# Kernel optimization log

Hardware: AMD Instinct MI355X
Metric: run time of the kernel (lower is better)

Reference implementation:

```python
import jax, jax.numpy as jnp
import numpy as np


def _l2norm(x, axis=1, eps=1e-12):
    n = jnp.sqrt(jnp.sum(x * x, axis=axis, keepdims=True))
    return x / jnp.maximum(n, eps)


def _update(query, keys, labels, class_counts, num_classes):
    # Vectorized form of Memory.update + get_update_query (train branch).
    m, d = keys.shape
    q = _l2norm(query, axis=1)                              # [N, d]
    score = q @ keys.T                                      # [N, m]
    s_q = jax.nn.softmax(score, axis=0)                     # softmax over queries
    s_m = jax.nn.softmax(score, axis=1)                     # softmax over memory slots
    gather = jnp.argmax(s_m, axis=1)                        # top-1 slot per query, [N]
    # per-slot scatter-reduce: sum_{i: argmax_i==j} s_q[i,j]/max_i s_q[i,j] * q[i]
    w = s_q / jnp.max(s_q, axis=0, keepdims=True)           # [N, m]
    onehot = (gather[:, None] == jnp.arange(m)[None, :]).astype(q.dtype)
    qu = (w * onehot).T @ q                                 # [m, d]
    part = m // num_classes
    slot_class = jnp.arange(m) // part                      # class id of each slot
    active = (slot_class[:, None] == labels[None, :]).any(axis=1)
    qu = jnp.where(active[:, None], qu, 0.0)                # only slots of present classes
    # count-weighted running-average update; torch loop overwrites
    # updated_keys_final each iteration, so only the LAST unique label
    # (torch.unique is sorted -> max) takes effect. Faithful to that.
    last = jnp.max(labels)
    count = jnp.sum(labels == last).astype(q.dtype)
    in_part = slot_class == last
    temp = jnp.where(in_part, class_counts[last], 1.0)[:, None]   # [m, 1]
    updated = temp * keys + qu
    temp2 = temp + jnp.where(in_part, count, 0.0)[:, None]
    return _l2norm(updated / temp2, axis=1)                 # [m, d]


def _read(embedding, mem, num_classes):
    # Memory.read: per-partition block_compare, score is detached in torch.
    m, d = mem.shape
    pr = m // (num_classes - 1)
    nblk = m // pr
    qr = embedding.reshape(d, -1).T                         # [Nq, d]
    blocks = mem.reshape(nblk, pr, d)

    def blk(b):
        s = jax.lax.stop_gradient(b @ qr.T)                 # [pr, Nq] (detached)
        return s.T @ b                                      # [Nq, d]

    return jax.vmap(blk)(blocks)                            # [nblk, Nq, d]


def setup_inputs():
    key = jax.random.key(0)
    k1, k2, k3, k4, k5 = jax.random.split(key, 5)
    N, d, m, C, Nq, L = 8192, 256, 4608, 9, 16384, 16
    return {
        "query": jax.random.normal(k1, (N, d), jnp.float32),
        "embeddings_src": jax.random.normal(k2, (d, Nq), jnp.float32),
        "embeddings_tgt": jax.random.normal(k3, (d, Nq), jnp.float32),
        "keys": _l2norm(jax.random.normal(k4, (m, d), jnp.float32), axis=1),
        "class_counts": jnp.ones((C,), jnp.float32),
        "labels": jax.random.randint(k5, (L,), 1, C).astype(jnp.int32),
        "num_classes": C,
    }


def reference(query, embeddings_src, embeddings_tgt, keys, class_counts, labels, num_classes):
    mem = _update(query, keys, labels, class_counts, num_classes)
    feat_src = _read(embeddings_src, mem, num_classes)
    feat_tgt = _read(embeddings_tgt, mem, num_classes)
    return jnp.stack([feat_src, feat_tgt])                  # [2, nblk, Nq, d]
```

## Files before the change

kernel.cpp:

```cpp
#include <hip/hip_runtime.h>
#include <math.h>

#define NQRY 8192
#define DIM  256
#define MS   4608
#define NQE  16384
#define NBLK 8
#define PRROWS 576

typedef __attribute__((ext_vector_type(8))) short bf16x8;
typedef __attribute__((ext_vector_type(4))) float f32x4;


__device__ __forceinline__ unsigned ordf(float f) {
  unsigned u = __float_as_uint(f);
  return (u & 0x80000000u) ? ~u : (u | 0x80000000u);
}
__device__ __forceinline__ float unordf(unsigned u) {
  unsigned b = (u & 0x80000000u) ? (u & 0x7FFFFFFFu) : ~u;
  return __uint_as_float(b);
}
__device__ __forceinline__ unsigned short bf16rn(float x) {
  unsigned u = __float_as_uint(x);
  unsigned r = u + 0x7FFFu + ((u >> 16) & 1u);
  return (unsigned short)(r >> 16);
}
__device__ __forceinline__ void splitbf(float x, unsigned short& h, unsigned short& lo) {
  unsigned u = __float_as_uint(x);
  h = (unsigned short)(u >> 16);
  float hf = __uint_as_float(u & 0xFFFF0000u);
  lo = bf16rn(x - hf);
}

__global__ __launch_bounds__(256) void k_zero(float4* __restrict__ p, int n4) {
  int i = blockIdx.x * 256 + threadIdx.x;
  if (i < n4) p[i] = float4{0.f, 0.f, 0.f, 0.f};
}

__global__ __launch_bounds__(256) void k_qnorm(const float* __restrict__ query,
                                               float* __restrict__ q,
                                               unsigned short* __restrict__ qh,
                                               unsigned short* __restrict__ ql) {
  int i = blockIdx.x, t = threadIdx.x;
  size_t idx = (size_t)i * DIM + t;
  float x = query[idx];
  float v = x * x;
  #pragma unroll
  for (int o = 32; o; o >>= 1) v += __shfl_down(v, o);
  __shared__ float s[4];
  if ((t & 63) == 0) s[t >> 6] = v;
  __syncthreads();
  float ss = (s[0] + s[1]) + (s[2] + s[3]);
  float qq = x / fmaxf(sqrtf(ss), 1e-12f);
  q[idx] = qq;
  unsigned short h, lo;
  splitbf(qq, h, lo);
  qh[idx] = h; ql[idx] = lo;
}

__global__ __launch_bounds__(256) void k_ksplit(const float* __restrict__ keys,
                                                unsigned short* __restrict__ kh,
                                                unsigned short* __restrict__ kl) {
  size_t idx = (size_t)blockIdx.x * 256 + threadIdx.x;
  unsigned short h, lo;
  splitbf(keys[idx], h, lo);
  kh[idx] = h; kl[idx] = lo;
}

__global__ __launch_bounds__(256) void k_embt(const float* __restrict__ embS,
                                              const float* __restrict__ embT,
                                              unsigned short* __restrict__ ebT) {
  __shared__ float tile[64][33];
  int z = blockIdx.z;
  const float* emb = z ? embT : embS;
  int n0 = blockIdx.x * 32, k0 = blockIdx.y * 64;
  int t = threadIdx.x;
  int kl = t >> 5, nl = t & 31;
  #pragma unroll
  for (int i = 0; i < 8; i++)
    tile[kl * 8 + i][nl] = emb[(size_t)(k0 + kl * 8 + i) * NQE + n0 + nl];
  __syncthreads();
  int nl2 = t >> 3, kq = (t & 7) * 8;
  bf16x8 hv;
  #pragma unroll
  for (int j = 0; j < 8; j++) hv[j] = (short)bf16rn(tile[kq + j][nl2]);
  *(bf16x8*)(ebT + (size_t)z * NQE * DIM + (size_t)(n0 + nl2) * DIM + k0 + kq) = hv;
}

__global__ void k_scalars(const int* __restrict__ labels,
                          const float* __restrict__ cc,
                          float* __restrict__ sc) {
  int t = threadIdx.x;
  int l = (t < 16) ? labels[t] : (int)0x80000000;
  int mx = l;
  #pragma unroll
  for (int o = 32; o; o >>= 1) mx = max(mx, __shfl_down(mx, o));
  mx = __shfl(mx, 0);
  int cnt = (t < 16 && l == mx) ? 1 : 0;
  #pragma unroll
  for (int o = 32; o; o >>= 1) cnt += __shfl_down(cnt, o);
  unsigned amv = (t < 16) ? (1u << l) : 0u;
  #pragma unroll
  for (int o = 32; o; o >>= 1) amv |= __shfl_down(amv, o);
  if (t == 0) {
    sc[0] = __int_as_float(mx);
    sc[1] = (float)cnt;
    sc[2] = cc[mx];
    sc[3] = __uint_as_float(amv);
  }
}

__global__ __launch_bounds__(256) void k_scoremax(
    const unsigned short* __restrict__ qh, const unsigned short* __restrict__ ql,
    const unsigned short* __restrict__ kh, const unsigned short* __restrict__ kl,
    unsigned long long* __restrict__ rowbest, unsigned* __restrict__ colmax) {
  __shared__ __align__(16) char smem[65536];
  char* sAh = smem;          char* sAl = smem + 16384;
  char* sBh = smem + 32768;  char* sBl = smem + 49152;
  int tid = threadIdx.x;
  int n0 = blockIdx.x * 128, m0 = blockIdx.y * 128;
  int w = tid >> 6, l = tid & 63;
  int wm = w >> 1, wn = w & 1;
  int lr = l >> 4, lc = l & 15;
  f32x4 acc[4][4] = {};
  for (int kk = 0; kk < 4; kk++) {
    __syncthreads();
    #pragma unroll
    for (int t = 0; t < 4; t++) {
      int c = t * 256 + tid;
      int row = c >> 3, cc = c & 7;
      int ldsb = row * 128 + ((cc * 16) ^ ((row & 7) << 4));
      size_t gA = (size_t)(m0 + row) * DIM + kk * 64 + cc * 8;
      size_t gB = (size_t)(n0 + row) * DIM + kk * 64 + cc * 8;
      *(bf16x8*)(sAh + ldsb) = *(const bf16x8*)(qh + gA);
      *(bf16x8*)(sAl + ldsb) = *(const bf16x8*)(ql + gA);
      *(bf16x8*)(sBh + ldsb) = *(const bf16x8*)(kh + gB);
      *(bf16x8*)(sBl + ldsb) = *(const bf16x8*)(kl + gB);
    }
    __syncthreads();
    #pragma unroll
    for (int st = 0; st < 2; st++) {
      bf16x8 ah[4], al[4], bh[4], bl[4];
      #pragma unroll
      for (int f = 0; f < 4; f++) {
        int ra = wm * 64 + f * 16 + lc;
        int ka = (st * 64 + lr * 16) ^ ((ra & 7) << 4);
        ah[f] = *(const bf16x8*)(sAh + ra * 128 + ka);
        al[f] = *(const bf16x8*)(sAl + ra * 128 + ka);
        int rb = wn * 64 + f * 16 + lc;
        int kb = (st * 64 + lr * 16) ^ ((rb & 7) << 4);
        bh[f] = *(const bf16x8*)(sBh + rb * 128 + kb);
        bl[f] = *(const bf16x8*)(sBl + rb * 128 + kb);
      }
      #pragma unroll
      for (int fm = 0; fm < 4; fm++)
        #pragma unroll
        for (int fn = 0; fn < 4; fn++) {
          acc[fm][fn] = __builtin_amdgcn_mfma_f32_16x16x32_bf16(ah[fm], bh[fn], acc[fm][fn], 0, 0, 0);
          acc[fm][fn] = __builtin_amdgcn_mfma_f32_16x16x32_bf16(ah[fm], bl[fn], acc[fm][fn], 0, 0, 0);
          acc[fm][fn] = __builtin_amdgcn_mfma_f32_16x16x32_bf16(al[fm], bh[fn], acc[fm][fn], 0, 0, 0);
        }
    }
  }
  #pragma unroll
  for (int fm = 0; fm < 4; fm++) {
    #pragma unroll
    for (int rg = 0; rg < 4; rg++) {
      unsigned long long p = 0ull;
      #pragma unroll
      for (int fn = 0; fn < 4; fn++) {
        float v = acc[fm][fn][rg];
        unsigned ng = (unsigned)(n0 + wn * 64 + fn * 16 + lc);
        unsigned long long cand =
            ((unsigned long long)ordf(v) << 32) | (unsigned long long)(0xFFFFFFFFu - ng);
        if (cand > p) p = cand;
      }
      #pragma unroll
      for (int o = 1; o < 16; o <<= 1) {
        unsigned long long t2 = __shfl_xor(p, o);
        if (t2 > p) p = t2;
      }
      if (lc == 0)
        atomicMax(rowbest + (m0 + wm * 64 + fm * 16 + lr * 4 + rg), p);
    }
  }
  #pragma unroll
  for (int fn = 0; fn < 4; fn++) {
    float v = -3.4e38f;
    #pragma unroll
    for (int fm = 0; fm < 4; fm++)
      #pragma unroll
      for (int rg = 0; rg < 4; rg++) v = fmaxf(v, acc[fm][fn][rg]);
    v = fmaxf(v, __shfl_xor(v, 16));
    v = fmaxf(v, __shfl_xor(v, 32));
    if (lr == 0) atomicMax(colmax + (n0 + wn * 64 + fn * 16 + lc), ordf(v));
  }
}

__global__ __launch_bounds__(256) void k_rowscatter(
    const unsigned long long* __restrict__ rowbest, const unsigned* __restrict__ colmax,
    const float* __restrict__ q, float* __restrict__ qu) {
  int i = blockIdx.x, t = threadIdx.x;
  unsigned long long p = rowbest[i];
  int g = (int)(0xFFFFFFFFu - (unsigned)(p & 0xFFFFFFFFull));
  float sv = unordf((unsigned)(p >> 32));
  float w = expf(sv - unordf(colmax[g]));
  atomicAdd(qu + (size_t)g * DIM + t, w * q[(size_t)i * DIM + t]);
}

__global__ __launch_bounds__(256) void k_mem(const float* __restrict__ keys,
                                             const float* __restrict__ qu,
                                             const float* __restrict__ sc,
                                             float* __restrict__ memr) {
  int j = blockIdx.x, t = threadIdx.x;
  int last = __float_as_int(sc[0]);
  float count = sc[1], ccl = sc[2];
  unsigned am = __float_as_uint(sc[3]);
  int cls = j >> 9;
  bool inp = (cls == last);
  float temp = inp ? ccl : 1.0f;
  float quv = ((am >> cls) & 1u) ? qu[(size_t)j * DIM + t] : 0.0f;
  float u = temp * keys[(size_t)j * DIM + t] + quv;
  float temp2 = temp + (inp ? count : 0.0f);
  float v = u / temp2;
  float vv = v * v;
  #pragma unroll
  for (int o = 32; o; o >>= 1) vv += __shfl_down(vv, o);
  __shared__ float s[4];
  if ((t & 63) == 0) s[t >> 6] = vv;
  __syncthreads();
  float ss = (s[0] + s[1]) + (s[2] + s[3]);
  memr[(size_t)j * DIM + t] = v / fmaxf(sqrtf(ss), 1e-12f);
}

__global__ __launch_bounds__(256) void k_gram(const float* __restrict__ memr,
                                              unsigned short* __restrict__ Gb) {
  __shared__ float As[16][64];
  __shared__ float Bs[16][64];
  int b = blockIdx.z;
  int kxc = blockIdx.x * 64;
  int kyr = blockIdx.y * 64;
  const float* Ab = memr + (size_t)b * PRROWS * DIM;
  int tid = threadIdx.x, tx = tid & 15, ty = tid >> 4;
  int lp = tid >> 4;
  int lk = (tid & 15) * 4;
  float acc[4][4] = {};
  for (int p0 = 0; p0 < PRROWS; p0 += 16) {
    float4 av = *(const float4*)(Ab + (size_t)(p0 + lp) * DIM + kyr + lk);
    float4 bv = *(const float4*)(Ab + (size_t)(p0 + lp) * DIM + kxc + lk);
    __syncthreads();
    *(float4*)&As[lp][lk] = av;
    *(float4*)&Bs[lp][lk] = bv;
    __syncthreads();
    #pragma unroll
    for (int p = 0; p < 16; p++) {
      float a[4], c[4];
      *(float4*)&a[0] = *(const float4*)&As[p][ty * 4];
      *(float4*)&c[0] = *(const float4*)&Bs[p][tx * 4];
      #pragma unroll
      for (int r = 0; r < 4; r++)
        #pragma unroll
        for (int s2 = 0; s2 < 4; s2++)
          acc[r][s2] = fmaf(a[r], c[s2], acc[r][s2]);
    }
  }
  #pragma unroll
  for (int r = 0; r < 4; r++)
    #pragma unroll
    for (int s2 = 0; s2 < 4; s2++)
      Gb[(size_t)b * DIM * DIM + (size_t)(kyr + ty * 4 + r) * DIM + kxc + tx * 4 + s2] =
          bf16rn(acc[r][s2]);
}

__global__ __launch_bounds__(256) void k_read_mfma(
    const unsigned short* __restrict__ ebT, const unsigned short* __restrict__ Gb,
    float* __restrict__ out) {
  __shared__ __align__(16) char smem[32768];
  char* sA = smem;
  char* sB = smem + 16384;
  int tid = threadIdx.x;
  int eb = blockIdx.z;
  const unsigned short* ea = ebT + (size_t)(eb >> 3) * NQE * DIM;
  const unsigned short* gb = Gb + (size_t)(eb & 7) * DIM * DIM;
  int n0 = blockIdx.x * 128, d0 = blockIdx.y * 128;
  int w = tid >> 6, l = tid & 63;
  int wm = w >> 1, wn = w & 1;
  int lr = l >> 4, lc = l & 15;
  f32x4 acc[4][4] = {};
  for (int kk = 0; kk < 4; kk++) {
    __syncthreads();
    #pragma unroll
    for (int t = 0; t < 4; t++) {
      int c = t * 256 + tid;
      int row = c >> 3, cc = c & 7;
      int ldsb = row * 128 + ((cc * 16) ^ ((row & 7) << 4));
      size_t gA = (size_t)(n0 + row) * DIM + kk * 64 + cc * 8;
      size_t gB = (size_t)(d0 + row) * DIM + kk * 64 + cc * 8;
      *(bf16x8*)(sA + ldsb) = *(const bf16x8*)(ea + gA);
      *(bf16x8*)(sB + ldsb) = *(const bf16x8*)(gb + gB);
    }
    __syncthreads();
    #pragma unroll
    for (int st = 0; st < 2; st++) {
      bf16x8 ah[4], bh[4];
      #pragma unroll
      for (int f = 0; f < 4; f++) {
        int ra = wm * 64 + f * 16 + lc;
        int ka = (st * 64 + lr * 16) ^ ((ra & 7) << 4);
        ah[f] = *(const bf16x8*)(sA + ra * 128 + ka);
        int rb = wn * 64 + f * 16 + lc;
        int kb = (st * 64 + lr * 16) ^ ((rb & 7) << 4);
        bh[f] = *(const bf16x8*)(sB + rb * 128 + kb);
      }
      #pragma unroll
      for (int fm = 0; fm < 4; fm++)
        #pragma unroll
        for (int fn = 0; fn < 4; fn++)
          acc[fm][fn] = __builtin_amdgcn_mfma_f32_16x16x32_bf16(ah[fm], bh[fn], acc[fm][fn], 0, 0, 0);
    }
  }
  size_t base = (size_t)eb * NQE * DIM;
  #pragma unroll
  for (int fm = 0; fm < 4; fm++)
    #pragma unroll
    for (int rg = 0; rg < 4; rg++) {
      int n = n0 + wm * 64 + fm * 16 + lr * 4 + rg;
      float* op = out + base + (size_t)n * DIM + d0 + wn * 64 + lc;
      #pragma unroll
      for (int fn = 0; fn < 4; fn++) op[fn * 16] = acc[fm][fn][rg];
    }
}

extern "C" void kernel_launch(void* const* d_in, const int* in_sizes, int n_in,
                              void* d_out, int out_size, void* d_ws, size_t ws_size,
                              hipStream_t stream) {
  const float* query  = (const float*)d_in[0];
  const float* embS   = (const float*)d_in[1];
  const float* embT   = (const float*)d_in[2];
  const float* keys   = (const float*)d_in[3];
  const float* cc     = (const float*)d_in[4];
  const int*   labels = (const int*)d_in[5];
  float* out = (float*)d_out;

  float* q                     = out;
  unsigned short* qh           = (unsigned short*)(out + 2097152);
  unsigned short* ql           = (unsigned short*)(out + 3145728);
  unsigned short* kh           = (unsigned short*)(out + 4194304);
  unsigned short* kl           = (unsigned short*)(out + 4784128);
  float* qu                    = out + 5373952;
  unsigned long long* rowbest  = (unsigned long long*)(out + 6553600);
  unsigned* colmax             = (unsigned*)(out + 6569984);
  float* memr                  = out + 6574592;

  unsigned short* ebT = (unsigned short*)d_ws;
  unsigned short* Gb  = (unsigned short*)((char*)d_ws + 16777216);
  float* sc           = (float*)((char*)d_ws + 17825792);

  const int n4 = (1179648 + 16384 + 4608) / 4;
  k_zero<<<(n4 + 255) / 256, 256, 0, stream>>>((float4*)qu, n4);

  k_qnorm<<<NQRY, 256, 0, stream>>>(query, q, qh, ql);
  k_ksplit<<<MS, 256, 0, stream>>>(keys, kh, kl);
  k_embt<<<dim3(NQE / 32, DIM / 64, 2), 256, 0, stream>>>(embS, embT, ebT);
  k_scalars<<<1, 64, 0, stream>>>(labels, cc, sc);
  k_scoremax<<<dim3(MS / 128, NQRY / 128), 256, 0, stream>>>(qh, ql, kh, kl, rowbest, colmax);
  k_rowscatter<<<NQRY, 256, 0, stream>>>(rowbest, colmax, q, qu);
  k_mem<<<MS, 256, 0, stream>>>(keys, qu, sc, memr);
  k_gram<<<dim3(4, 4, NBLK), 256, 0, stream>>>(memr, Gb);
  k_read_mfma<<<dim3(NQE / 128, DIM / 128, 2 * NBLK), 256, 0, stream>>>(ebT, Gb, out);
}
```

Baseline: 236.2 us.

## Concatenate split-bf16 operands along K and swizzle block order in scoremax

```diff
diff --git a/kernel.cpp b/kernel.cpp
--- a/kernel.cpp
+++ b/kernel.cpp
@@ -7,6 +7,7 @@
 #define NQE  16384
 #define NBLK 8
 #define PRROWS 576
+#define KEFF 768
 
 typedef __attribute__((ext_vector_type(8))) short bf16x8;
 typedef __attribute__((ext_vector_type(4))) float f32x4;
@@ -39,8 +40,7 @@
 
 __global__ __launch_bounds__(256) void k_qnorm(const float* __restrict__ query,
                                                float* __restrict__ q,
-                                               unsigned short* __restrict__ qh,
-                                               unsigned short* __restrict__ ql) {
+                                               unsigned short* __restrict__ A2) {
   int i = blockIdx.x, t = threadIdx.x;
   size_t idx = (size_t)i * DIM + t;
   float x = query[idx];
@@ -55,16 +55,17 @@
   q[idx] = qq;
   unsigned short h, lo;
   splitbf(qq, h, lo);
-  qh[idx] = h; ql[idx] = lo;
+  size_t r = (size_t)i * KEFF + t;
+  A2[r] = h; A2[r + 256] = lo; A2[r + 512] = h;
 }
 
 __global__ __launch_bounds__(256) void k_ksplit(const float* __restrict__ keys,
-                                                unsigned short* __restrict__ kh,
-                                                unsigned short* __restrict__ kl) {
-  size_t idx = (size_t)blockIdx.x * 256 + threadIdx.x;
+                                                unsigned short* __restrict__ B2) {
+  int j = blockIdx.x, t = threadIdx.x;
   unsigned short h, lo;
-  splitbf(keys[idx], h, lo);
-  kh[idx] = h; kl[idx] = lo;
+  splitbf(keys[(size_t)j * DIM + t], h, lo);
+  size_t r = (size_t)j * KEFF + t;
+  B2[r] = h; B2[r + 256] = h; B2[r + 512] = lo;
 }
 
 __global__ __launch_bounds__(256) void k_embt(const float* __restrict__ embS,
@@ -111,55 +112,50 @@
 }
 
 __global__ __launch_bounds__(256) void k_scoremax(
-    const unsigned short* __restrict__ qh, const unsigned short* __restrict__ ql,
-    const unsigned short* __restrict__ kh, const unsigned short* __restrict__ kl,
+    const unsigned short* __restrict__ A2, const unsigned short* __restrict__ B2,
     unsigned long long* __restrict__ rowbest, unsigned* __restrict__ colmax) {
-  __shared__ __align__(16) char smem[65536];
-  char* sAh = smem;          char* sAl = smem + 16384;
-  char* sBh = smem + 32768;  char* sBl = smem + 49152;
+  __shared__ __align__(16) char smem[32768];
+  char* sA = smem;
+  char* sB = smem + 16384;
   int tid = threadIdx.x;
-  int n0 = blockIdx.x * 128, m0 = blockIdx.y * 128;
-  int w = tid >> 6, l = tid & 63;
+  int bid = blockIdx.x;
+  int swz = (bid & 7) * 288 + (bid >> 3);
+  int bx = swz % 36, by = swz / 36;
+  int n0 = bx * 128, m0 = by * 128;
+  int w = tid >> 6, lane = tid & 63;
   int wm = w >> 1, wn = w & 1;
-  int lr = l >> 4, lc = l & 15;
+  int lr = lane >> 4, lc = lane & 15;
   f32x4 acc[4][4] = {};
-  for (int kk = 0; kk < 4; kk++) {
+  for (int kk = 0; kk < 12; kk++) {
     __syncthreads();
     #pragma unroll
     for (int t = 0; t < 4; t++) {
       int c = t * 256 + tid;
       int row = c >> 3, cc = c & 7;
       int ldsb = row * 128 + ((cc * 16) ^ ((row & 7) << 4));
-      size_t gA = (size_t)(m0 + row) * DIM + kk * 64 + cc * 8;
-      size_t gB = (size_t)(n0 + row) * DIM + kk * 64 + cc * 8;
-      *(bf16x8*)(sAh + ldsb) = *(const bf16x8*)(qh + gA);
-      *(bf16x8*)(sAl + ldsb) = *(const bf16x8*)(ql + gA);
-      *(bf16x8*)(sBh + ldsb) = *(const bf16x8*)(kh + gB);
-      *(bf16x8*)(sBl + ldsb) = *(const bf16x8*)(kl + gB);
+      *(bf16x8*)(sA + ldsb) =
+          *(const bf16x8*)(A2 + (size_t)(m0 + row) * KEFF + kk * 64 + cc * 8);
+      *(bf16x8*)(sB + ldsb) =
+          *(const bf16x8*)(B2 + (size_t)(n0 + row) * KEFF + kk * 64 + cc * 8);
     }
     __syncthreads();
     #pragma unroll
     for (int st = 0; st < 2; st++) {
-      bf16x8 ah[4], al[4], bh[4], bl[4];
+      bf16x8 af[4], bf[4];
       #pragma unroll
       for (int f = 0; f < 4; f++) {
         int ra = wm * 64 + f * 16 + lc;
         int ka = (st * 64 + lr * 16) ^ ((ra & 7) << 4);
-        ah[f] = *(const bf16x8*)(sAh + ra * 128 + ka);
-        al[f] = *(const bf16x8*)(sAl + ra * 128 + ka);
+        af[f] = *(const bf16x8*)(sA + ra * 128 + ka);
         int rb = wn * 64 + f * 16 + lc;
         int kb = (st * 64 + lr * 16) ^ ((rb & 7) << 4);
-        bh[f] = *(const bf16x8*)(sBh + rb * 128 + kb);
-        bl[f] = *(const bf16x8*)(sBl + rb * 128 + kb);
+        bf[f] = *(const bf16x8*)(sB + rb * 128 + kb);
       }
       #pragma unroll
       for (int fm = 0; fm < 4; fm++)
         #pragma unroll
-        for (int fn = 0; fn < 4; fn++) {
-          acc[fm][fn] = __builtin_amdgcn_mfma_f32_16x16x32_bf16(ah[fm], bh[fn], acc[fm][fn], 0, 0, 0);
-          acc[fm][fn] = __builtin_amdgcn_mfma_f32_16x16x32_bf16(ah[fm], bl[fn], acc[fm][fn], 0, 0, 0);
-          acc[fm][fn] = __builtin_amdgcn_mfma_f32_16x16x32_bf16(al[fm], bh[fn], acc[fm][fn], 0, 0, 0);
-        }
+        for (int fn = 0; fn < 4; fn++)
+          acc[fm][fn] = __builtin_amdgcn_mfma_f32_16x16x32_bf16(af[fm], bf[fn], acc[fm][fn], 0, 0, 0);
     }
   }
   #pragma unroll
@@ -302,21 +298,21 @@
     __syncthreads();
     #pragma unroll
     for (int st = 0; st < 2; st++) {
-      bf16x8 ah[4], bh[4];
+      bf16x8 af[4], bf[4];
       #pragma unroll
       for (int f = 0; f < 4; f++) {
         int ra = wm * 64 + f * 16 + lc;
         int ka = (st * 64 + lr * 16) ^ ((ra & 7) << 4);
-        ah[f] = *(const bf16x8*)(sA + ra * 128 + ka);
+        af[f] = *(const bf16x8*)(sA + ra * 128 + ka);
         int rb = wn * 64 + f * 16 + lc;
         int kb = (st * 64 + lr * 16) ^ ((rb & 7) << 4);
-        bh[f] = *(const bf16x8*)(sB + rb * 128 + kb);
+        bf[f] = *(const bf16x8*)(sB + rb * 128 + kb);
       }
       #pragma unroll
       for (int fm = 0; fm < 4; fm++)
         #pragma unroll
         for (int fn = 0; fn < 4; fn++)
-          acc[fm][fn] = __builtin_amdgcn_mfma_f32_16x16x32_bf16(ah[fm], bh[fn], acc[fm][fn], 0, 0, 0);
+          acc[fm][fn] = __builtin_amdgcn_mfma_f32_16x16x32_bf16(af[fm], bf[fn], acc[fm][fn], 0, 0, 0);
     }
   }
   size_t base = (size_t)eb * NQE * DIM;
@@ -343,14 +339,12 @@
   float* out = (float*)d_out;
 
   float* q                     = out;
-  unsigned short* qh           = (unsigned short*)(out + 2097152);
-  unsigned short* ql           = (unsigned short*)(out + 3145728);
-  unsigned short* kh           = (unsigned short*)(out + 4194304);
-  unsigned short* kl           = (unsigned short*)(out + 4784128);
-  float* qu                    = out + 5373952;
-  unsigned long long* rowbest  = (unsigned long long*)(out + 6553600);
-  unsigned* colmax             = (unsigned*)(out + 6569984);
-  float* memr                  = out + 6574592;
+  unsigned short* A2           = (unsigned short*)(out + 2097152);
+  unsigned short* B2           = (unsigned short*)(out + 5242880);
+  float* qu                    = out + 7012352;
+  unsigned long long* rowbest  = (unsigned long long*)(out + 8192000);
+  unsigned* colmax             = (unsigned*)(out + 8208384);
+  float* memr                  = out + 8212992;
 
   unsigned short* ebT = (unsigned short*)d_ws;
   unsigned short* Gb  = (unsigned short*)((char*)d_ws + 16777216);
@@ -359,11 +353,11 @@
   const int n4 = (1179648 + 16384 + 4608) / 4;
   k_zero<<<(n4 + 255) / 256, 256, 0, stream>>>((float4*)qu, n4);
 
-  k_qnorm<<<NQRY, 256, 0, stream>>>(query, q, qh, ql);
-  k_ksplit<<<MS, 256, 0, stream>>>(keys, kh, kl);
+  k_qnorm<<<NQRY, 256, 0, stream>>>(query, q, A2);
+  k_ksplit<<<MS, 256, 0, stream>>>(keys, B2);
   k_embt<<<dim3(NQE / 32, DIM / 64, 2), 256, 0, stream>>>(embS, embT, ebT);
   k_scalars<<<1, 64, 0, stream>>>(labels, cc, sc);
-  k_scoremax<<<dim3(MS / 128, NQRY / 128), 256, 0, stream>>>(qh, ql, kh, kl, rowbest, colmax);
+  k_scoremax<<<64 * 36, 256, 0, stream>>>(A2, B2, rowbest, colmax);
   k_rowscatter<<<NQRY, 256, 0, stream>>>(rowbest, colmax, q, qu);
   k_mem<<<MS, 256, 0, stream>>>(keys, qu, sc, memr);
   k_gram<<<dim3(4, 4, NBLK), 256, 0, stream>>>(memr, Gb);
```

Result: slower. 281.6 us (+19.2%).

## Halve LDS in split-bf16 score GEMM by packing hi/lo into shared tiles

Applied to the files above, without the earlier changes.

```diff
diff --git a/kernel.cpp b/kernel.cpp
--- a/kernel.cpp
+++ b/kernel.cpp
@@ -114,51 +114,54 @@
     const unsigned short* __restrict__ qh, const unsigned short* __restrict__ ql,
     const unsigned short* __restrict__ kh, const unsigned short* __restrict__ kl,
     unsigned long long* __restrict__ rowbest, unsigned* __restrict__ colmax) {
-  __shared__ __align__(16) char smem[65536];
-  char* sAh = smem;          char* sAl = smem + 16384;
-  char* sBh = smem + 32768;  char* sBl = smem + 49152;
+  __shared__ __align__(16) char smem[32768];
+  char* sA = smem;
+  char* sB = smem + 16384;
   int tid = threadIdx.x;
   int n0 = blockIdx.x * 128, m0 = blockIdx.y * 128;
-  int w = tid >> 6, l = tid & 63;
+  int w = tid >> 6, lane = tid & 63;
   int wm = w >> 1, wn = w & 1;
-  int lr = l >> 4, lc = l & 15;
+  int lr = lane >> 4, lc = lane & 15;
+  int srow = tid >> 3, sc8 = tid & 7;
   f32x4 acc[4][4] = {};
-  for (int kk = 0; kk < 4; kk++) {
-    __syncthreads();
-    #pragma unroll
-    for (int t = 0; t < 4; t++) {
-      int c = t * 256 + tid;
-      int row = c >> 3, cc = c & 7;
-      int ldsb = row * 128 + ((cc * 16) ^ ((row & 7) << 4));
-      size_t gA = (size_t)(m0 + row) * DIM + kk * 64 + cc * 8;
-      size_t gB = (size_t)(n0 + row) * DIM + kk * 64 + cc * 8;
-      *(bf16x8*)(sAh + ldsb) = *(const bf16x8*)(qh + gA);
-      *(bf16x8*)(sAl + ldsb) = *(const bf16x8*)(ql + gA);
-      *(bf16x8*)(sBh + ldsb) = *(const bf16x8*)(kh + gB);
-      *(bf16x8*)(sBl + ldsb) = *(const bf16x8*)(kl + gB);
-    }
-    __syncthreads();
-    #pragma unroll
-    for (int st = 0; st < 2; st++) {
-      bf16x8 ah[4], al[4], bh[4], bl[4];
-      #pragma unroll
-      for (int f = 0; f < 4; f++) {
-        int ra = wm * 64 + f * 16 + lc;
-        int ka = (st * 64 + lr * 16) ^ ((ra & 7) << 4);
-        ah[f] = *(const bf16x8*)(sAh + ra * 128 + ka);
-        al[f] = *(const bf16x8*)(sAl + ra * 128 + ka);
-        int rb = wn * 64 + f * 16 + lc;
-        int kb = (st * 64 + lr * 16) ^ ((rb & 7) << 4);
-        bh[f] = *(const bf16x8*)(sBh + rb * 128 + kb);
-        bl[f] = *(const bf16x8*)(sBl + rb * 128 + kb);
+  for (int kk = 0; kk < 8; kk++) {
+    __syncthreads();
+    #pragma unroll
+    for (int t = 0; t < 8; t++) {
+      int row = (t & 3) * 32 + srow;
+      const unsigned short* hi = (t < 4) ? qh : kh;
+      const unsigned short* lo = (t < 4) ? ql : kl;
+      int base = (t < 4) ? m0 : n0;
+      const unsigned short* src =
+          ((sc8 < 4) ? hi : lo) + (size_t)(base + row) * DIM + kk * 32 + (sc8 & 3) * 8;
+      char* dst = ((t < 4) ? sA : sB) + row * 128 + ((sc8 ^ (row & 7)) << 4);
+      *(bf16x8*)dst = *(const bf16x8*)src;
+    }
+    __syncthreads();
+    bf16x8 ah[4], al[4];
+    #pragma unroll
+    for (int f = 0; f < 4; f++) {
+      int ra = wm * 64 + f * 16 + lc;
+      ah[f] = *(const bf16x8*)(sA + ra * 128 + ((lr ^ (ra & 7)) << 4));
+      al[f] = *(const bf16x8*)(sA + ra * 128 + (((lr + 4) ^ (ra & 7)) << 4));
+    }
+    #pragma unroll
+    for (int half = 0; half < 2; half++) {
+      bf16x8 bh[2], bl[2];
+      #pragma unroll
+      for (int f2 = 0; f2 < 2; f2++) {
+        int rb = wn * 64 + (half * 2 + f2) * 16 + lc;
+        bh[f2] = *(const bf16x8*)(sB + rb * 128 + ((lr ^ (rb & 7)) << 4));
+        bl[f2] = *(const bf16x8*)(sB + rb * 128 + (((lr + 4) ^ (rb & 7)) << 4));
       }
       #pragma unroll
       for (int fm = 0; fm < 4; fm++)
         #pragma unroll
-        for (int fn = 0; fn < 4; fn++) {
-          acc[fm][fn] = __builtin_amdgcn_mfma_f32_16x16x32_bf16(ah[fm], bh[fn], acc[fm][fn], 0, 0, 0);
-          acc[fm][fn] = __builtin_amdgcn_mfma_f32_16x16x32_bf16(ah[fm], bl[fn], acc[fm][fn], 0, 0, 0);
-          acc[fm][fn] = __builtin_amdgcn_mfma_f32_16x16x32_bf16(al[fm], bh[fn], acc[fm][fn], 0, 0, 0);
+        for (int f2 = 0; f2 < 2; f2++) {
+          int fn = half * 2 + f2;
+          acc[fm][fn] = __builtin_amdgcn_mfma_f32_16x16x32_bf16(ah[fm], bh[f2], acc[fm][fn], 0, 0, 0);
+          acc[fm][fn] = __builtin_amdgcn_mfma_f32_16x16x32_bf16(ah[fm], bl[f2], acc[fm][fn], 0, 0, 0);
+          acc[fm][fn] = __builtin_amdgcn_mfma_f32_16x16x32_bf16(al[fm], bh[f2], acc[fm][fn], 0, 0, 0);
         }
     }
   }
@@ -302,21 +305,21 @@
     __syncthreads();
     #pragma unroll
     for (int st = 0; st < 2; st++) {
-      bf16x8 ah[4], bh[4];
+      bf16x8 af[4], bf[4];
       #pragma unroll
       for (int f = 0; f < 4; f++) {
         int ra = wm * 64 + f * 16 + lc;
         int ka = (st * 64 + lr * 16) ^ ((ra & 7) << 4);
-        ah[f] = *(const bf16x8*)(sA + ra * 128 + ka);
+        af[f] = *(const bf16x8*)(sA + ra * 128 + ka);
         int rb = wn * 64 + f * 16 + lc;
         int kb = (st * 64 + lr * 16) ^ ((rb & 7) << 4);
-        bh[f] = *(const bf16x8*)(sB + rb * 128 + kb);
+        bf[f] = *(const bf16x8*)(sB + rb * 128 + kb);
       }
       #pragma unroll
       for (int fm = 0; fm < 4; fm++)
         #pragma unroll
         for (int fn = 0; fn < 4; fn++)
-          acc[fm][fn] = __builtin_amdgcn_mfma_f32_16x16x32_bf16(ah[fm], bh[fn], acc[fm][fn], 0, 0, 0);
+          acc[fm][fn] = __builtin_amdgcn_mfma_f32_16x16x32_bf16(af[fm], bf[fn], acc[fm][fn], 0, 0, 0);
     }
   }
   size_t base = (size_t)eb * NQE * DIM;
```

Measured after the change: 227.3 us. 1.04x faster.
